# Optimization experiments

Measured on AMD Instinct MI355X. Metric: run time of the kernel, lower is better.

Reference implementation:

```python
import jax, jax.numpy as jnp
import numpy as np

ALPHA = 0.1
K = 5


def setup_inputs() -> dict:
    key = jax.random.key(0)
    ks = jax.random.split(key, 6)
    N, E = 50000, 800000
    IN, HID, OUT = 512, 256, 64
    x = jax.random.normal(ks[0], (N, IN), dtype=jnp.float32)
    edge_index = jax.random.randint(ks[1], (2, E), 0, N, dtype=jnp.int64)
    # Linear params (torch Linear: y = x @ W.T + b), kaiming-ish scale
    W1 = jax.random.normal(ks[2], (HID, IN), dtype=jnp.float32) / np.sqrt(IN)
    b1 = jnp.zeros((HID,), dtype=jnp.float32)
    W2 = jax.random.normal(ks[3], (OUT, HID), dtype=jnp.float32) / np.sqrt(HID)
    b2 = jnp.zeros((OUT,), dtype=jnp.float32)
    return {"x": x, "W1": W1, "b1": b1, "W2": W2, "b2": b2,
            "edge_index": edge_index}


def reference(x, W1, b1, W2, b2, edge_index):
    N = x.shape[0]
    # --- MLP encoder (eval mode: dropout is identity) ---
    h = jax.nn.relu(x @ W1.T + b1)          # [N, HID]
    h = h @ W2.T + b2                       # [N, OUT]

    # --- gcn_norm with self-loops (PyG APPNP default) ---
    src, dst = edge_index[0], edge_index[1]
    loop = jnp.arange(N, dtype=src.dtype)
    src_f = jnp.concatenate([src, loop])    # [E+N]
    dst_f = jnp.concatenate([dst, loop])
    ew = jnp.ones(src_f.shape[0], dtype=h.dtype)
    deg = jax.ops.segment_sum(ew, dst_f, num_segments=N)
    dinv = jnp.where(deg > 0, jax.lax.rsqrt(deg), 0.0)
    norm = dinv[src_f] * dinv[dst_f]        # [E+N]

    # --- K iterations of personalized-PageRank propagation ---
    def body(xk, _):
        msg = norm[:, None] * xk[src_f]                      # gather [E+N, OUT]
        agg = jax.ops.segment_sum(msg, dst_f, num_segments=N)
        return (1.0 - ALPHA) * agg + ALPHA * h, None

    xK, _ = jax.lax.scan(body, h, None, length=K)
    return jax.nn.log_softmax(xK, axis=1)
```

## Files before the change

### kernel.cpp

```cpp
#include <hip/hip_runtime.h>
#include <hip/hip_bf16.h>

#define IN_DIM  512
#define HID_DIM 256
#define OUT_DIM 64

typedef __attribute__((ext_vector_type(8))) short bf16x8;
typedef __attribute__((ext_vector_type(4))) float f32x4;

static __device__ __forceinline__ ushort f2b(float f) {
    __hip_bfloat16 b = __float2bfloat16(f);
    return *reinterpret_cast<ushort*>(&b);
}
static __device__ __forceinline__ float b2f_lo(uint u) {
    union { uint u; float f; } t; t.u = u << 16; return t.f;
}
static __device__ __forceinline__ float b2f_hi(uint u) {
    union { uint u; float f; } t; t.u = u & 0xFFFF0000u; return t.f;
}
static __device__ __forceinline__ uint packbf(float x, float y) {
    return (uint)f2b(x) | ((uint)f2b(y) << 16);
}

#define GLOAD16(g, l) __builtin_amdgcn_global_load_lds(                      \
    (const __attribute__((address_space(1))) void*)(g),                      \
    (__attribute__((address_space(3))) void*)(l), 16, 0, 0)


__global__ __launch_bounds__(256) void f2b_kernel(const float* __restrict__ in,
                                                  ushort* __restrict__ out, int n8) {
    for (int i = blockIdx.x * 256 + threadIdx.x; i < n8; i += gridDim.x * 256) {
        float4 a = *reinterpret_cast<const float4*>(&in[(size_t)i * 8]);
        float4 b = *reinterpret_cast<const float4*>(&in[(size_t)i * 8 + 4]);
        ushort4 lo = make_ushort4(f2b(a.x), f2b(a.y), f2b(a.z), f2b(a.w));
        ushort4 hi = make_ushort4(f2b(b.x), f2b(b.y), f2b(b.z), f2b(b.w));
        *reinterpret_cast<ushort4*>(&out[(size_t)i * 8])     = lo;
        *reinterpret_cast<ushort4*>(&out[(size_t)i * 8 + 4]) = hi;
    }
}


__global__ void hist_kernel(const int* __restrict__ ei, int* __restrict__ deg, int E) {
    int e = blockIdx.x * 256 + threadIdx.x;
    if (e < E) atomicAdd(&deg[ei[E + e]], 1);
}

__global__ __launch_bounds__(256) void scanA_kernel(const int* __restrict__ deg,
                                                    int* __restrict__ offs,
                                                    int* __restrict__ bsum, int N) {
    __shared__ int sh[256];
    int tid = threadIdx.x;
    int i = blockIdx.x * 256 + tid;
    int v = (i < N) ? deg[i] : 0;
    sh[tid] = v;
    __syncthreads();
#pragma unroll
    for (int off = 1; off < 256; off <<= 1) {
        int t = (tid >= off) ? sh[tid - off] : 0;
        __syncthreads();
        sh[tid] += t;
        __syncthreads();
    }
    if (i < N) offs[i] = sh[tid] - v;
    if (tid == 255) bsum[blockIdx.x] = sh[255];
}

__global__ __launch_bounds__(256) void scanB_kernel(int* __restrict__ bsum, int nb) {
    __shared__ int sh[256];
    int tid = threadIdx.x;
    int v = (tid < nb) ? bsum[tid] : 0;
    sh[tid] = v;
    __syncthreads();
#pragma unroll
    for (int off = 1; off < 256; off <<= 1) {
        int t = (tid >= off) ? sh[tid - off] : 0;
        __syncthreads();
        sh[tid] += t;
        __syncthreads();
    }
    if (tid < nb) bsum[tid] = sh[tid] - v;
}

__global__ __launch_bounds__(256) void scanC_kernel(const int* __restrict__ deg,
                                                    const int* __restrict__ bsum,
                                                    int* __restrict__ offs,
                                                    float* __restrict__ dinv,
                                                    int N, int E) {
    int i = blockIdx.x * 256 + threadIdx.x;
    if (i < N) {
        offs[i] += bsum[i >> 8];
        dinv[i] = rsqrtf((float)(deg[i] + 1));
    }
    if (i == 0) offs[N] = E;
}

__global__ void fill_kernel(const int* __restrict__ ei, const int* __restrict__ offs,
                            int* __restrict__ cursor, const float* __restrict__ dinv,
                            uint* __restrict__ edat, int E) {
    int e = blockIdx.x * 256 + threadIdx.x;
    if (e < E) {
        int s = ei[e];
        int d = ei[E + e];
        int pos = offs[d] + atomicAdd(&cursor[d], 1);
        edat[pos] = (uint)s | ((uint)f2b(dinv[d] * dinv[s]) << 16);
    }
}


__global__ __launch_bounds__(256) void gemm1_f32a(const float* __restrict__ A,
                                                  const ushort* __restrict__ B,
                                                  const float* __restrict__ bias,
                                                  ushort* __restrict__ C, int M) {
    constexpr int K = IN_DIM;
    constexpr int NK = K / 32;
    __shared__ float  Asf[2][128 * 32];
    __shared__ ushort Bs[2][128 * 32];

    const int tid  = threadIdx.x;
    const int lane = tid & 63;
    const int wid  = tid >> 6;
    const int wm = wid >> 1, wn = wid & 1;
    const int m0 = blockIdx.y * 128;
    const int n0 = blockIdx.x * 128;
    const int l15 = lane & 15;
    const int lq  = lane >> 4;

    const int a_row  = lane >> 3;
    const int a_slot = (lane & 7) ^ a_row;
    const int b_row  = lane >> 2;
    const int b_slot = (lane & 3) ^ ((lane >> 3) & 3);

    f32x4 acc[4][4];
#pragma unroll
    for (int i = 0; i < 4; ++i)
#pragma unroll
        for (int j = 0; j < 4; ++j) acc[i][j] = (f32x4)0.0f;

    auto stage = [&](int buf, int ks) {
        const int k0 = ks * 32;
#pragma unroll
        for (int q = 0; q < 4; ++q) {
            const int rbase = (wid * 4 + q) * 8;
            int am = m0 + rbase + a_row; if (am >= M) am = M - 1;
            const float* ga = A + (size_t)am * K + k0 + a_slot * 4;
            GLOAD16(ga, &Asf[buf][rbase * 32]);
        }
#pragma unroll
        for (int q = 0; q < 2; ++q) {
            const int rbase = (wid * 2 + q) * 16;
            const int row = rbase + b_row;
            const ushort* gb = B + (size_t)(n0 + row) * K + k0 + b_slot * 8;
            GLOAD16(gb, &Bs[buf][rbase * 32]);
        }
    };

    stage(0, 0);
    __syncthreads();

#pragma unroll 2
    for (int ks = 0; ks < NK; ++ks) {
        const int cur = ks & 1;
        if (ks + 1 < NK) stage(cur ^ 1, ks + 1);

        bf16x8 af[4], bf[4];
#pragma unroll
        for (int f = 0; f < 4; ++f) {
            const int ar = wm * 64 + f * 16 + l15;
            const int r7 = ar & 7;
            f32x4 v0 = *reinterpret_cast<const f32x4*>(&Asf[cur][ar * 32 + (((2 * lq) ^ r7) << 2)]);
            f32x4 v1 = *reinterpret_cast<const f32x4*>(&Asf[cur][ar * 32 + (((2 * lq + 1) ^ r7) << 2)]);
            bf16x8 a;
            a[0] = (short)f2b(v0[0]); a[1] = (short)f2b(v0[1]);
            a[2] = (short)f2b(v0[2]); a[3] = (short)f2b(v0[3]);
            a[4] = (short)f2b(v1[0]); a[5] = (short)f2b(v1[1]);
            a[6] = (short)f2b(v1[2]); a[7] = (short)f2b(v1[3]);
            af[f] = a;
            const int br = wn * 64 + f * 16 + l15;
            bf[f] = *reinterpret_cast<const bf16x8*>(&Bs[cur][br * 32 + ((lq ^ ((br >> 1) & 3)) << 3)]);
        }
#pragma unroll
        for (int i = 0; i < 4; ++i)
#pragma unroll
            for (int j = 0; j < 4; ++j)
                acc[i][j] = __builtin_amdgcn_mfma_f32_16x16x32_bf16(af[i], bf[j], acc[i][j], 0, 0, 0);

        __syncthreads();
    }

    const int lr = lq * 4;
#pragma unroll
    for (int nf = 0; nf < 4; ++nf) {
        int col = n0 + wn * 64 + nf * 16 + l15;
        float bv = bias[col];
#pragma unroll
        for (int mf = 0; mf < 4; ++mf) {
#pragma unroll
            for (int j = 0; j < 4; ++j) {
                int row = m0 + wm * 64 + mf * 16 + lr + j;
                if (row < M) {
                    float v = fmaxf(acc[mf][nf][j] + bv, 0.f);
                    C[(size_t)row * HID_DIM + col] = f2b(v);
                }
            }
        }
    }
}


#define LDT 40

__global__ __launch_bounds__(256) void gemm2_bf16(const ushort* __restrict__ A,
                                                  const float* __restrict__ B,
                                                  const float* __restrict__ bias,
                                                  ushort* __restrict__ Cb,
                                                  int M) {
    constexpr int K = HID_DIM;
    constexpr int NK = K / 32;
    __shared__ ushort As[128 * LDT];
    __shared__ ushort Bs[64 * LDT];

    const int tid = threadIdx.x;
    const int lane = tid & 63;
    const int wid = tid >> 6;
    const int wm = wid >> 1, wn = wid & 1;
    const int m0 = blockIdx.x * 128;
    const int l15 = lane & 15;
    const int koff = (lane >> 4) * 8;

    f32x4 acc[4][2];
#pragma unroll
    for (int i = 0; i < 4; ++i)
#pragma unroll
        for (int j = 0; j < 2; ++j) acc[i][j] = (f32x4)0.0f;

    uint4 rawA[2];
    float4 rbv[2];
#pragma unroll
    for (int i = 0; i < 2; ++i) {
        int slot = tid + i * 256;
        int rowA = slot >> 2, c8 = (slot & 3) << 3;
        int m = m0 + rowA;
        rawA[i] = (m < M) ? *reinterpret_cast<const uint4*>(&A[(size_t)m * K + c8])
                          : make_uint4(0u, 0u, 0u, 0u);
        int rowB = slot >> 3, c4 = (slot & 7) << 2;
        rbv[i] = *reinterpret_cast<const float4*>(&B[(size_t)rowB * K + c4]);
    }
#pragma unroll
    for (int i = 0; i < 2; ++i) {
        int slot = tid + i * 256;
        int rowA = slot >> 2, c8 = (slot & 3) << 3;
        *reinterpret_cast<uint4*>(&As[rowA * LDT + c8]) = rawA[i];
        int rowB = slot >> 3, c4 = (slot & 7) << 2;
        ushort4 ub = make_ushort4(f2b(rbv[i].x), f2b(rbv[i].y), f2b(rbv[i].z), f2b(rbv[i].w));
        *reinterpret_cast<ushort4*>(&Bs[rowB * LDT + c4]) = ub;
    }
    __syncthreads();

    for (int ks = 0; ks < NK; ++ks) {
        if (ks + 1 < NK) {
            int k0 = (ks + 1) * 32;
#pragma unroll
            for (int i = 0; i < 2; ++i) {
                int slot = tid + i * 256;
                int rowA = slot >> 2, c8 = (slot & 3) << 3;
                int m = m0 + rowA;
                rawA[i] = (m < M) ? *reinterpret_cast<const uint4*>(&A[(size_t)m * K + k0 + c8])
                                  : make_uint4(0u, 0u, 0u, 0u);
                int rowB = slot >> 3, c4 = (slot & 7) << 2;
                rbv[i] = *reinterpret_cast<const float4*>(&B[(size_t)rowB * K + k0 + c4]);
            }
        }
        bf16x8 af[4], bf[2];
#pragma unroll
        for (int f = 0; f < 4; ++f)
            af[f] = *reinterpret_cast<const bf16x8*>(&As[(wm * 64 + f * 16 + l15) * LDT + koff]);
#pragma unroll
        for (int f = 0; f < 2; ++f)
            bf[f] = *reinterpret_cast<const bf16x8*>(&Bs[(wn * 32 + f * 16 + l15) * LDT + koff]);
#pragma unroll
        for (int i = 0; i < 4; ++i)
#pragma unroll
            for (int j = 0; j < 2; ++j)
                acc[i][j] = __builtin_amdgcn_mfma_f32_16x16x32_bf16(af[i], bf[j], acc[i][j], 0, 0, 0);
        __syncthreads();
        if (ks + 1 < NK) {
#pragma unroll
            for (int i = 0; i < 2; ++i) {
                int slot = tid + i * 256;
                int rowA = slot >> 2, c8 = (slot & 3) << 3;
                *reinterpret_cast<uint4*>(&As[rowA * LDT + c8]) = rawA[i];
                int rowB = slot >> 3, c4 = (slot & 7) << 2;
                ushort4 ub = make_ushort4(f2b(rbv[i].x), f2b(rbv[i].y), f2b(rbv[i].z), f2b(rbv[i].w));
                *reinterpret_cast<ushort4*>(&Bs[rowB * LDT + c4]) = ub;
            }
            __syncthreads();
        }
    }

    const int lr = (lane >> 4) * 4;
#pragma unroll
    for (int nf = 0; nf < 2; ++nf) {
        int col = wn * 32 + nf * 16 + l15;
        float bv = bias[col];
#pragma unroll
        for (int mf = 0; mf < 4; ++mf) {
#pragma unroll
            for (int j = 0; j < 4; ++j) {
                int row = m0 + wm * 64 + mf * 16 + lr + j;
                if (row < M)
                    Cb[(size_t)row * OUT_DIM + col] = f2b(acc[mf][nf][j] + bv);
            }
        }
    }
}


__global__ __launch_bounds__(256) void propb_kernel(const uint* __restrict__ xin,
                                                    const uint* __restrict__ hb,
                                                    const float* __restrict__ dinv,
                                                    const int* __restrict__ offs,
                                                    const uint* __restrict__ edat,
                                                    uint* __restrict__ xout, int N) {
    int node = blockIdx.x * 8 + (threadIdx.x >> 5);
    int l32 = threadIdx.x & 31;
    if (node >= N) return;
    int e0 = offs[node], e1 = offs[node + 1];

    float ax[4] = {0.f, 0.f, 0.f, 0.f};
    float ay[4] = {0.f, 0.f, 0.f, 0.f};
    int e = e0;
    for (; e + 8 <= e1; e += 8) {
        uint p0 = edat[e+0], p1 = edat[e+1], p2 = edat[e+2], p3 = edat[e+3];
        uint p4 = edat[e+4], p5 = edat[e+5], p6 = edat[e+6], p7 = edat[e+7];
        uint g0 = xin[(size_t)(p0 & 0xFFFFu) * 32 + l32];
        uint g1 = xin[(size_t)(p1 & 0xFFFFu) * 32 + l32];
        uint g2 = xin[(size_t)(p2 & 0xFFFFu) * 32 + l32];
        uint g3 = xin[(size_t)(p3 & 0xFFFFu) * 32 + l32];
        uint g4 = xin[(size_t)(p4 & 0xFFFFu) * 32 + l32];
        uint g5 = xin[(size_t)(p5 & 0xFFFFu) * 32 + l32];
        uint g6 = xin[(size_t)(p6 & 0xFFFFu) * 32 + l32];
        uint g7 = xin[(size_t)(p7 & 0xFFFFu) * 32 + l32];
        ax[0] = fmaf(b2f_hi(p0), b2f_lo(g0), ax[0]); ay[0] = fmaf(b2f_hi(p0), b2f_hi(g0), ay[0]);
        ax[1] = fmaf(b2f_hi(p1), b2f_lo(g1), ax[1]); ay[1] = fmaf(b2f_hi(p1), b2f_hi(g1), ay[1]);
        ax[2] = fmaf(b2f_hi(p2), b2f_lo(g2), ax[2]); ay[2] = fmaf(b2f_hi(p2), b2f_hi(g2), ay[2]);
        ax[3] = fmaf(b2f_hi(p3), b2f_lo(g3), ax[3]); ay[3] = fmaf(b2f_hi(p3), b2f_hi(g3), ay[3]);
        ax[0] = fmaf(b2f_hi(p4), b2f_lo(g4), ax[0]); ay[0] = fmaf(b2f_hi(p4), b2f_hi(g4), ay[0]);
        ax[1] = fmaf(b2f_hi(p5), b2f_lo(g5), ax[1]); ay[1] = fmaf(b2f_hi(p5), b2f_hi(g5), ay[1]);
        ax[2] = fmaf(b2f_hi(p6), b2f_lo(g6), ax[2]); ay[2] = fmaf(b2f_hi(p6), b2f_hi(g6), ay[2]);
        ax[3] = fmaf(b2f_hi(p7), b2f_lo(g7), ax[3]); ay[3] = fmaf(b2f_hi(p7), b2f_hi(g7), ay[3]);
    }
    for (; e < e1; ++e) {
        uint p = edat[e];
        uint g = xin[(size_t)(p & 0xFFFFu) * 32 + l32];
        ax[0] = fmaf(b2f_hi(p), b2f_lo(g), ax[0]);
        ay[0] = fmaf(b2f_hi(p), b2f_hi(g), ay[0]);
    }
    float sx = (ax[0] + ax[1]) + (ax[2] + ax[3]);
    float sy = (ay[0] + ay[1]) + (ay[2] + ay[3]);
    float di = dinv[node];
    uint gs = xin[(size_t)node * 32 + l32];
    sx = fmaf(di * di, b2f_lo(gs), sx);
    sy = fmaf(di * di, b2f_hi(gs), sy);
    uint ah = hb[(size_t)node * 32 + l32];
    float r0 = 0.9f * sx + 0.1f * b2f_lo(ah);
    float r1 = 0.9f * sy + 0.1f * b2f_hi(ah);
    xout[(size_t)node * 32 + l32] = packbf(r0, r1);
}


__global__ __launch_bounds__(256) void propb_lsm_kernel(const uint* __restrict__ xin,
                                                        const uint* __restrict__ hb,
                                                        const float* __restrict__ dinv,
                                                        const int* __restrict__ offs,
                                                        const uint* __restrict__ edat,
                                                        float* __restrict__ out, int N) {
    int node = blockIdx.x * 8 + (threadIdx.x >> 5);
    int l32 = threadIdx.x & 31;
    if (node >= N) return;
    int e0 = offs[node], e1 = offs[node + 1];

    float ax[4] = {0.f, 0.f, 0.f, 0.f};
    float ay[4] = {0.f, 0.f, 0.f, 0.f};
    int e = e0;
    for (; e + 8 <= e1; e += 8) {
        uint p0 = edat[e+0], p1 = edat[e+1], p2 = edat[e+2], p3 = edat[e+3];
        uint p4 = edat[e+4], p5 = edat[e+5], p6 = edat[e+6], p7 = edat[e+7];
        uint g0 = xin[(size_t)(p0 & 0xFFFFu) * 32 + l32];
        uint g1 = xin[(size_t)(p1 & 0xFFFFu) * 32 + l32];
        uint g2 = xin[(size_t)(p2 & 0xFFFFu) * 32 + l32];
        uint g3 = xin[(size_t)(p3 & 0xFFFFu) * 32 + l32];
        uint g4 = xin[(size_t)(p4 & 0xFFFFu) * 32 + l32];
        uint g5 = xin[(size_t)(p5 & 0xFFFFu) * 32 + l32];
        uint g6 = xin[(size_t)(p6 & 0xFFFFu) * 32 + l32];
        uint g7 = xin[(size_t)(p7 & 0xFFFFu) * 32 + l32];
        ax[0] = fmaf(b2f_hi(p0), b2f_lo(g0), ax[0]); ay[0] = fmaf(b2f_hi(p0), b2f_hi(g0), ay[0]);
        ax[1] = fmaf(b2f_hi(p1), b2f_lo(g1), ax[1]); ay[1] = fmaf(b2f_hi(p1), b2f_hi(g1), ay[1]);
        ax[2] = fmaf(b2f_hi(p2), b2f_lo(g2), ax[2]); ay[2] = fmaf(b2f_hi(p2), b2f_hi(g2), ay[2]);
        ax[3] = fmaf(b2f_hi(p3), b2f_lo(g3), ax[3]); ay[3] = fmaf(b2f_hi(p3), b2f_hi(g3), ay[3]);
        ax[0] = fmaf(b2f_hi(p4), b2f_lo(g4), ax[0]); ay[0] = fmaf(b2f_hi(p4), b2f_hi(g4), ay[0]);
        ax[1] = fmaf(b2f_hi(p5), b2f_lo(g5), ax[1]); ay[1] = fmaf(b2f_hi(p5), b2f_hi(g5), ay[1]);
        ax[2] = fmaf(b2f_hi(p6), b2f_lo(g6), ax[2]); ay[2] = fmaf(b2f_hi(p6), b2f_hi(g6), ay[2]);
        ax[3] = fmaf(b2f_hi(p7), b2f_lo(g7), ax[3]); ay[3] = fmaf(b2f_hi(p7), b2f_hi(g7), ay[3]);
    }
    for (; e < e1; ++e) {
        uint p = edat[e];
        uint g = xin[(size_t)(p & 0xFFFFu) * 32 + l32];
        ax[0] = fmaf(b2f_hi(p), b2f_lo(g), ax[0]);
        ay[0] = fmaf(b2f_hi(p), b2f_hi(g), ay[0]);
    }
    float sx = (ax[0] + ax[1]) + (ax[2] + ax[3]);
    float sy = (ay[0] + ay[1]) + (ay[2] + ay[3]);
    float di = dinv[node];
    uint gs = xin[(size_t)node * 32 + l32];
    sx = fmaf(di * di, b2f_lo(gs), sx);
    sy = fmaf(di * di, b2f_hi(gs), sy);
    uint ah = hb[(size_t)node * 32 + l32];
    float r0 = 0.9f * sx + 0.1f * b2f_lo(ah);
    float r1 = 0.9f * sy + 0.1f * b2f_hi(ah);

    float m = fmaxf(r0, r1);
    for (int o = 16; o > 0; o >>= 1) m = fmaxf(m, __shfl_xor(m, o));
    float sum = expf(r0 - m) + expf(r1 - m);
    for (int o = 16; o > 0; o >>= 1) sum += __shfl_xor(sum, o);
    float ls = logf(sum);
    float2 o2 = make_float2(r0 - m - ls, r1 - m - ls);
    *reinterpret_cast<float2*>(&out[(size_t)node * 64 + l32 * 2]) = o2;
}


static inline size_t align256(size_t x) { return (x + 255) & ~(size_t)255; }

extern "C" void kernel_launch(void* const* d_in, const int* in_sizes, int n_in,
                              void* d_out, int out_size, void* d_ws, size_t ws_size,
                              hipStream_t stream) {
    const float* x  = (const float*)d_in[0];
    const float* W1 = (const float*)d_in[1];
    const float* b1 = (const float*)d_in[2];
    const float* W2 = (const float*)d_in[3];
    const float* b2 = (const float*)d_in[4];
    const int*   ei = (const int*)d_in[5];

    const int N = in_sizes[0] / IN_DIM;
    const int E = in_sizes[5] / 2;
    const int nb = (N + 255) / 256;

    char* base = (char*)d_ws;
    size_t off = 0;
    uint*  hb  = (uint*)(base + off);    off += align256((size_t)N * 32 * 4);
    uint*  xsa = (uint*)(base + off);    off += align256((size_t)N * 32 * 4);
    uint*  xsb = (uint*)(base + off);    off += align256((size_t)N * 32 * 4);
    ushort* w1b = (ushort*)(base + off); off += align256((size_t)HID_DIM * IN_DIM * 2);
    ushort* h1  = (ushort*)(base + off); off += align256((size_t)N * HID_DIM * 2);
    float* dinv = (float*)(base + off);  off += align256((size_t)N * 4);
    int*   deg  = (int*)(base + off);    off += align256((size_t)N * 4);
    int*   offs = (int*)(base + off);    off += align256((size_t)(N + 1) * 4);
    int*   cur  = (int*)(base + off);    off += align256((size_t)N * 4);
    int*   bsum = (int*)(base + off);    off += align256((size_t)nb * 4);
    uint*  edat = (uint*)(base + off);   off += align256((size_t)E * 4);

    hipMemsetAsync(deg, 0, (size_t)N * 4, stream);
    hipMemsetAsync(cur, 0, (size_t)N * 4, stream);
    hist_kernel<<<(E + 255) / 256, 256, 0, stream>>>(ei, deg, E);
    scanA_kernel<<<nb, 256, 0, stream>>>(deg, offs, bsum, N);
    scanB_kernel<<<1, 256, 0, stream>>>(bsum, nb);
    scanC_kernel<<<nb, 256, 0, stream>>>(deg, bsum, offs, dinv, N, E);
    fill_kernel<<<(E + 255) / 256, 256, 0, stream>>>(ei, offs, cur, dinv, edat, E);

    f2b_kernel<<<64, 256, 0, stream>>>(W1, w1b, HID_DIM * IN_DIM / 8);

    {
        dim3 g(HID_DIM / 128, (N + 127) / 128);
        gemm1_f32a<<<g, 256, 0, stream>>>(x, w1b, b1, h1, N);
    }
    {
        dim3 g((N + 127) / 128);
        gemm2_bf16<<<g, 256, 0, stream>>>(h1, W2, b2, (ushort*)hb, N);
    }

    int blocks = (N + 7) / 8;
    propb_kernel<<<blocks, 256, 0, stream>>>(hb,  hb, dinv, offs, edat, xsa, N);
    propb_kernel<<<blocks, 256, 0, stream>>>(xsa, hb, dinv, offs, edat, xsb, N);
    propb_kernel<<<blocks, 256, 0, stream>>>(xsb, hb, dinv, offs, edat, xsa, N);
    propb_kernel<<<blocks, 256, 0, stream>>>(xsa, hb, dinv, offs, edat, xsb, N);
    propb_lsm_kernel<<<blocks, 256, 0, stream>>>(xsb, hb, dinv, offs, edat,
                                                 (float*)d_out, N);
}
```

Before: 284.4 us.

## Drop GEMM1 LDS double-buffering and widen propagation gather unroll to 16

The first GEMM goes from a double-buffered LDS pipeline to a single buffer: each k-step loads its tile, synchronizes, then computes. This halves shared-memory use, which may raise occupancy, but loads no longer overlap with MFMA work. The propagation kernels now issue 16 edge gathers per iteration instead of 8, with a 4-wide remainder loop, to keep more memory requests in flight. This costs more registers per thread.

```diff
diff --git a/kernel.cpp b/kernel.cpp
--- a/kernel.cpp
+++ b/kernel.cpp
@@ -113,8 +113,8 @@
                                                   ushort* __restrict__ C, int M) {
     constexpr int K = IN_DIM;
     constexpr int NK = K / 32;
-    __shared__ float  Asf[2][128 * 32];
-    __shared__ ushort Bs[2][128 * 32];
+    __shared__ float  Asf[128 * 32];
+    __shared__ ushort Bs[128 * 32];
 
     const int tid  = threadIdx.x;
     const int lane = tid & 63;
@@ -136,39 +136,31 @@
 #pragma unroll
         for (int j = 0; j < 4; ++j) acc[i][j] = (f32x4)0.0f;
 
-    auto stage = [&](int buf, int ks) {
+    for (int ks = 0; ks < NK; ++ks) {
         const int k0 = ks * 32;
 #pragma unroll
         for (int q = 0; q < 4; ++q) {
             const int rbase = (wid * 4 + q) * 8;
             int am = m0 + rbase + a_row; if (am >= M) am = M - 1;
             const float* ga = A + (size_t)am * K + k0 + a_slot * 4;
-            GLOAD16(ga, &Asf[buf][rbase * 32]);
+            GLOAD16(ga, &Asf[rbase * 32]);
         }
 #pragma unroll
         for (int q = 0; q < 2; ++q) {
             const int rbase = (wid * 2 + q) * 16;
             const int row = rbase + b_row;
             const ushort* gb = B + (size_t)(n0 + row) * K + k0 + b_slot * 8;
-            GLOAD16(gb, &Bs[buf][rbase * 32]);
-        }
-    };
-
-    stage(0, 0);
-    __syncthreads();
-
-#pragma unroll 2
-    for (int ks = 0; ks < NK; ++ks) {
-        const int cur = ks & 1;
-        if (ks + 1 < NK) stage(cur ^ 1, ks + 1);
+            GLOAD16(gb, &Bs[rbase * 32]);
+        }
+        __syncthreads();
 
         bf16x8 af[4], bf[4];
 #pragma unroll
         for (int f = 0; f < 4; ++f) {
             const int ar = wm * 64 + f * 16 + l15;
             const int r7 = ar & 7;
-            f32x4 v0 = *reinterpret_cast<const f32x4*>(&Asf[cur][ar * 32 + (((2 * lq) ^ r7) << 2)]);
-            f32x4 v1 = *reinterpret_cast<const f32x4*>(&Asf[cur][ar * 32 + (((2 * lq + 1) ^ r7) << 2)]);
+            f32x4 v0 = *reinterpret_cast<const f32x4*>(&Asf[ar * 32 + (((2 * lq) ^ r7) << 2)]);
+            f32x4 v1 = *reinterpret_cast<const f32x4*>(&Asf[ar * 32 + (((2 * lq + 1) ^ r7) << 2)]);
             bf16x8 a;
             a[0] = (short)f2b(v0[0]); a[1] = (short)f2b(v0[1]);
             a[2] = (short)f2b(v0[2]); a[3] = (short)f2b(v0[3]);
@@ -176,7 +168,7 @@
             a[6] = (short)f2b(v1[2]); a[7] = (short)f2b(v1[3]);
             af[f] = a;
             const int br = wn * 64 + f * 16 + l15;
-            bf[f] = *reinterpret_cast<const bf16x8*>(&Bs[cur][br * 32 + ((lq ^ ((br >> 1) & 3)) << 3)]);
+            bf[f] = *reinterpret_cast<const bf16x8*>(&Bs[br * 32 + ((lq ^ ((br >> 1) & 3)) << 3)]);
         }
 #pragma unroll
         for (int i = 0; i < 4; ++i)
@@ -329,25 +321,31 @@
     float ax[4] = {0.f, 0.f, 0.f, 0.f};
     float ay[4] = {0.f, 0.f, 0.f, 0.f};
     int e = e0;
-    for (; e + 8 <= e1; e += 8) {
-        uint p0 = edat[e+0], p1 = edat[e+1], p2 = edat[e+2], p3 = edat[e+3];
-        uint p4 = edat[e+4], p5 = edat[e+5], p6 = edat[e+6], p7 = edat[e+7];
-        uint g0 = xin[(size_t)(p0 & 0xFFFFu) * 32 + l32];
-        uint g1 = xin[(size_t)(p1 & 0xFFFFu) * 32 + l32];
-        uint g2 = xin[(size_t)(p2 & 0xFFFFu) * 32 + l32];
-        uint g3 = xin[(size_t)(p3 & 0xFFFFu) * 32 + l32];
-        uint g4 = xin[(size_t)(p4 & 0xFFFFu) * 32 + l32];
-        uint g5 = xin[(size_t)(p5 & 0xFFFFu) * 32 + l32];
-        uint g6 = xin[(size_t)(p6 & 0xFFFFu) * 32 + l32];
-        uint g7 = xin[(size_t)(p7 & 0xFFFFu) * 32 + l32];
-        ax[0] = fmaf(b2f_hi(p0), b2f_lo(g0), ax[0]); ay[0] = fmaf(b2f_hi(p0), b2f_hi(g0), ay[0]);
-        ax[1] = fmaf(b2f_hi(p1), b2f_lo(g1), ax[1]); ay[1] = fmaf(b2f_hi(p1), b2f_hi(g1), ay[1]);
-        ax[2] = fmaf(b2f_hi(p2), b2f_lo(g2), ax[2]); ay[2] = fmaf(b2f_hi(p2), b2f_hi(g2), ay[2]);
-        ax[3] = fmaf(b2f_hi(p3), b2f_lo(g3), ax[3]); ay[3] = fmaf(b2f_hi(p3), b2f_hi(g3), ay[3]);
-        ax[0] = fmaf(b2f_hi(p4), b2f_lo(g4), ax[0]); ay[0] = fmaf(b2f_hi(p4), b2f_hi(g4), ay[0]);
-        ax[1] = fmaf(b2f_hi(p5), b2f_lo(g5), ax[1]); ay[1] = fmaf(b2f_hi(p5), b2f_hi(g5), ay[1]);
-        ax[2] = fmaf(b2f_hi(p6), b2f_lo(g6), ax[2]); ay[2] = fmaf(b2f_hi(p6), b2f_hi(g6), ay[2]);
-        ax[3] = fmaf(b2f_hi(p7), b2f_lo(g7), ax[3]); ay[3] = fmaf(b2f_hi(p7), b2f_hi(g7), ay[3]);
+    for (; e + 16 <= e1; e += 16) {
+        uint p[16], g[16];
+#pragma unroll
+        for (int i = 0; i < 16; ++i) p[i] = edat[e + i];
+#pragma unroll
+        for (int i = 0; i < 16; ++i) g[i] = xin[(size_t)(p[i] & 0xFFFFu) * 32 + l32];
+#pragma unroll
+        for (int i = 0; i < 16; ++i) {
+            float wgt = b2f_hi(p[i]);
+            ax[i & 3] = fmaf(wgt, b2f_lo(g[i]), ax[i & 3]);
+            ay[i & 3] = fmaf(wgt, b2f_hi(g[i]), ay[i & 3]);
+        }
+    }
+    for (; e + 4 <= e1; e += 4) {
+        uint p[4], g[4];
+#pragma unroll
+        for (int i = 0; i < 4; ++i) p[i] = edat[e + i];
+#pragma unroll
+        for (int i = 0; i < 4; ++i) g[i] = xin[(size_t)(p[i] & 0xFFFFu) * 32 + l32];
+#pragma unroll
+        for (int i = 0; i < 4; ++i) {
+            float wgt = b2f_hi(p[i]);
+            ax[i] = fmaf(wgt, b2f_lo(g[i]), ax[i]);
+            ay[i] = fmaf(wgt, b2f_hi(g[i]), ay[i]);
+        }
     }
     for (; e < e1; ++e) {
         uint p = edat[e];
@@ -382,25 +380,31 @@
     float ax[4] = {0.f, 0.f, 0.f, 0.f};
     float ay[4] = {0.f, 0.f, 0.f, 0.f};
     int e = e0;
-    for (; e + 8 <= e1; e += 8) {
-        uint p0 = edat[e+0], p1 = edat[e+1], p2 = edat[e+2], p3 = edat[e+3];
-        uint p4 = edat[e+4], p5 = edat[e+5], p6 = edat[e+6], p7 = edat[e+7];
-        uint g0 = xin[(size_t)(p0 & 0xFFFFu) * 32 + l32];
-        uint g1 = xin[(size_t)(p1 & 0xFFFFu) * 32 + l32];
-        uint g2 = xin[(size_t)(p2 & 0xFFFFu) * 32 + l32];
-        uint g3 = xin[(size_t)(p3 & 0xFFFFu) * 32 + l32];
-        uint g4 = xin[(size_t)(p4 & 0xFFFFu) * 32 + l32];
-        uint g5 = xin[(size_t)(p5 & 0xFFFFu) * 32 + l32];
-        uint g6 = xin[(size_t)(p6 & 0xFFFFu) * 32 + l32];
-        uint g7 = xin[(size_t)(p7 & 0xFFFFu) * 32 + l32];
-        ax[0] = fmaf(b2f_hi(p0), b2f_lo(g0), ax[0]); ay[0] = fmaf(b2f_hi(p0), b2f_hi(g0), ay[0]);
-        ax[1] = fmaf(b2f_hi(p1), b2f_lo(g1), ax[1]); ay[1] = fmaf(b2f_hi(p1), b2f_hi(g1), ay[1]);
-        ax[2] = fmaf(b2f_hi(p2), b2f_lo(g2), ax[2]); ay[2] = fmaf(b2f_hi(p2), b2f_hi(g2), ay[2]);
-        ax[3] = fmaf(b2f_hi(p3), b2f_lo(g3), ax[3]); ay[3] = fmaf(b2f_hi(p3), b2f_hi(g3), ay[3]);
-        ax[0] = fmaf(b2f_hi(p4), b2f_lo(g4), ax[0]); ay[0] = fmaf(b2f_hi(p4), b2f_hi(g4), ay[0]);
-        ax[1] = fmaf(b2f_hi(p5), b2f_lo(g5), ax[1]); ay[1] = fmaf(b2f_hi(p5), b2f_hi(g5), ay[1]);
-        ax[2] = fmaf(b2f_hi(p6), b2f_lo(g6), ax[2]); ay[2] = fmaf(b2f_hi(p6), b2f_hi(g6), ay[2]);
-        ax[3] = fmaf(b2f_hi(p7), b2f_lo(g7), ax[3]); ay[3] = fmaf(b2f_hi(p7), b2f_hi(g7), ay[3]);
+    for (; e + 16 <= e1; e += 16) {
+        uint p[16], g[16];
+#pragma unroll
+        for (int i = 0; i < 16; ++i) p[i] = edat[e + i];
+#pragma unroll
+        for (int i = 0; i < 16; ++i) g[i] = xin[(size_t)(p[i] & 0xFFFFu) * 32 + l32];
+#pragma unroll
+        for (int i = 0; i < 16; ++i) {
+            float wgt = b2f_hi(p[i]);
+            ax[i & 3] = fmaf(wgt, b2f_lo(g[i]), ax[i & 3]);
+            ay[i & 3] = fmaf(wgt, b2f_hi(g[i]), ay[i & 3]);
+        }
+    }
+    for (; e + 4 <= e1; e += 4) {
+        uint p[4], g[4];
+#pragma unroll
+        for (int i = 0; i < 4; ++i) p[i] = edat[e + i];
+#pragma unroll
+        for (int i = 0; i < 4; ++i) g[i] = xin[(size_t)(p[i] & 0xFFFFu) * 32 + l32];
+#pragma unroll
+        for (int i = 0; i < 4; ++i) {
+            float wgt = b2f_hi(p[i]);
+            ax[i] = fmaf(wgt, b2f_lo(g[i]), ax[i]);
+            ay[i] = fmaf(wgt, b2f_hi(g[i]), ay[i]);
+        }
     }
     for (; e < e1; ++e) {
         uint p = edat[e];
```

Result: no change. 278.9 us (-1.9%).
